# Kernel optimization log

Hardware: AMD Instinct MI355X
Metric: run time of the kernel (lower is better)

Reference implementation:

```python
import jax, jax.numpy as jnp
import numpy as np

EMBED = 128
HIDDEN = 256
N_NODES = 50000
N_EDGES = 640000
LN_EPS = 1e-5


def setup_inputs() -> dict:
    key = jax.random.key(0)
    ks = jax.random.split(key, 10)
    node_embeddings = jax.random.normal(ks[0], (N_NODES, EMBED), dtype=jnp.float32)
    edge_embeddings = jax.random.normal(ks[1], (N_EDGES, EMBED), dtype=jnp.float32)
    edge_index_list = jax.random.randint(ks[2], (2, N_EDGES), 0, N_NODES, dtype=jnp.int64 if jax.config.jax_enable_x64 else jnp.int32)
    # LayerNorm params
    ln_gamma = jnp.ones((EMBED,), dtype=jnp.float32)
    ln_beta = jnp.zeros((EMBED,), dtype=jnp.float32)
    # phi: Linear(embed->hidden), Linear(hidden->embed); xavier-ish init
    W1 = jax.random.normal(ks[3], (EMBED, HIDDEN), dtype=jnp.float32) * (1.0 / np.sqrt(EMBED))
    b1 = jnp.zeros((HIDDEN,), dtype=jnp.float32)
    W2 = jax.random.normal(ks[4], (HIDDEN, EMBED), dtype=jnp.float32) * (1.0 / np.sqrt(HIDDEN))
    b2 = jnp.zeros((EMBED,), dtype=jnp.float32)
    # theta: Linear(embed->embed)
    Wt = jax.random.normal(ks[5], (EMBED, EMBED), dtype=jnp.float32) * (1.0 / np.sqrt(EMBED))
    bt = jnp.zeros((EMBED,), dtype=jnp.float32)
    return {
        "node_embeddings": node_embeddings,
        "edge_embeddings": edge_embeddings,
        "edge_index_list": edge_index_list,
        "ln_gamma": ln_gamma, "ln_beta": ln_beta,
        "W1": W1, "b1": b1, "W2": W2, "b2": b2,
        "Wt": Wt, "bt": bt,
    }


def _layer_norm(x, gamma, beta):
    mu = jnp.mean(x, axis=-1, keepdims=True)
    var = jnp.var(x, axis=-1, keepdims=True)
    return (x - mu) * jax.lax.rsqrt(var + LN_EPS) * gamma + beta


def reference(node_embeddings, edge_embeddings, edge_index_list,
              ln_gamma, ln_beta, W1, b1, W2, b2, Wt, bt):
    n_nodes = node_embeddings.shape[0]
    h = _layer_norm(node_embeddings, ln_gamma, ln_beta)  # [N, D]
    center = edge_index_list[0]    # [E]
    neighbor = edge_index_list[1]  # [E]
    h_c = h[center]                # [E, D] gather
    h_n = h[neighbor]              # [E, D] gather
    s = edge_embeddings + h_c + h_n  # [E, D]
    # phi: SiLU -> Linear -> SiLU -> Linear
    t = jax.nn.silu(s) @ W1 + b1          # [E, H]
    theta_edge = jax.nn.silu(t) @ W2 + b2  # [E, D]
    msg = h_n * theta_edge                 # [E, D]
    agg = jax.ops.segment_sum(msg, center, num_segments=n_nodes)  # [N, D]
    # theta: SiLU -> Linear
    out = jax.nn.silu(h + agg) @ Wt + bt   # [N, D]
    return out
```

## Files before the change

kernel.cpp:

```cpp
#include <hip/hip_runtime.h>
#include <stdint.h>

#define EMBED 128
#define HIDDEN 256

typedef __bf16 v8bf __attribute__((ext_vector_type(8)));
typedef float v4f __attribute__((ext_vector_type(4)));

__device__ __forceinline__ float bf2f(unsigned short u){
    union { uint32_t i; float f; } v; v.i = ((uint32_t)u) << 16; return v.f;
}
__device__ __forceinline__ unsigned short f2bf(float f){
    union { float f; uint32_t i; } v; v.f = f;
    uint32_t i = v.i;
    uint32_t r = (i + 0x7fffu + ((i >> 16) & 1u)) >> 16;
    return (unsigned short)r;
}
__device__ __forceinline__ float lo_f(uint32_t u){ union{uint32_t i;float f;}v; v.i=u<<16; return v.f; }
__device__ __forceinline__ float hi_f(uint32_t u){ union{uint32_t i;float f;}v; v.i=u&0xffff0000u; return v.f; }
__device__ __forceinline__ uint32_t pack2(float a, float b){
    return (uint32_t)f2bf(a) | ((uint32_t)f2bf(b) << 16);
}
__device__ __forceinline__ float silu_f(float x){ return x / (1.0f + __expf(-x)); }

__device__ __forceinline__ float loadf(const void* b, size_t i, int isf32){
    return isf32 ? ((const float*)b)[i] : bf2f(((const unsigned short*)b)[i]);
}
__device__ __forceinline__ void load8f(const void* base, size_t off, int isf32, float o[8]){
    if (isf32){
        const float* p = (const float*)base + off;
        float4 a = *(const float4*)p, b = *(const float4*)(p + 4);
        o[0]=a.x;o[1]=a.y;o[2]=a.z;o[3]=a.w;o[4]=b.x;o[5]=b.y;o[6]=b.z;o[7]=b.w;
    } else {
        uint4 v = *(const uint4*)((const unsigned short*)base + off);
        uint32_t w[4] = {v.x, v.y, v.z, v.w};
        #pragma unroll
        for (int q = 0; q < 4; q++){ o[2*q] = lo_f(w[q]); o[2*q+1] = hi_f(w[q]); }
    }
}
__device__ __forceinline__ int idx_c(const int* ei, int e, int is64){
    return is64 ? ei[2*(size_t)e] : ei[e];
}
__device__ __forceinline__ int idx_n(const int* ei, int e, int E, int is64){
    return is64 ? ei[2*((size_t)E + e)] : ei[(size_t)E + e];
}

__global__ __launch_bounds__(256) void probe_kernel(
    const unsigned short* __restrict__ ne, const int* __restrict__ ei, int* __restrict__ flags)
{
    __shared__ int s_badf, s_nzidx;
    if (threadIdx.x == 0){ s_badf = 0; s_nzidx = 0; }
    __syncthreads();
    int t = threadIdx.x;
    int bad = 0;
    #pragma unroll
    for (int i = 0; i < 16; i++){
        unsigned short u = ne[t * 16 + i];
        int ex = (u >> 7) & 0xFF;
        if (ex >= 0x85) bad = 1;
    }
    if (bad) atomicOr(&s_badf, 1);
    if (t < 128 && ei[2 * t + 1] != 0) atomicOr(&s_nzidx, 1);
    __syncthreads();
    if (threadIdx.x == 0){ flags[0] = s_badf; flags[1] = s_nzidx ? 0 : 1; }
}

__global__ __launch_bounds__(256) void ln_kernel(
    const void* __restrict__ x, const void* __restrict__ g, const void* __restrict__ b,
    unsigned short* __restrict__ h, int N, const int* __restrict__ flags)
{
    int isf32 = flags[0];
    int wave = threadIdx.x >> 6, lane = threadIdx.x & 63;
    int node = blockIdx.x * 4 + wave;
    if (node >= N) return;
    float x0, x1;
    if (isf32){
        float2 v = *(const float2*)((const float*)x + (size_t)node * EMBED + lane * 2);
        x0 = v.x; x1 = v.y;
    } else {
        uint32_t u = *(const uint32_t*)((const unsigned short*)x + (size_t)node * EMBED + lane * 2);
        x0 = lo_f(u); x1 = hi_f(u);
    }
    float s = x0 + x1, ss = x0 * x0 + x1 * x1;
    for (int m = 1; m < 64; m <<= 1){ s += __shfl_xor(s, m); ss += __shfl_xor(ss, m); }
    float mean = s * (1.0f / EMBED);
    float var  = ss * (1.0f / EMBED) - mean * mean;
    float rs   = rsqrtf(var + 1e-5f);
    float g0 = loadf(g, lane * 2, isf32), g1 = loadf(g, lane * 2 + 1, isf32);
    float b0 = loadf(b, lane * 2, isf32), b1v = loadf(b, lane * 2 + 1, isf32);
    float y0 = (x0 - mean) * rs * g0 + b0;
    float y1 = (x1 - mean) * rs * g1 + b1v;
    *(uint32_t*)(h + (size_t)node * EMBED + lane * 2) = pack2(y0, y1);
}

__global__ __launch_bounds__(256) void prepack_kernel(
    const void* __restrict__ W1, const void* __restrict__ W2, const void* __restrict__ Wt,
    const void* __restrict__ b1, const void* __restrict__ b2, const void* __restrict__ bt,
    unsigned short* __restrict__ W1p, unsigned short* __restrict__ W2p,
    unsigned short* __restrict__ Wtp, unsigned short* __restrict__ bpk,
    const int* __restrict__ flags)
{
    int isf32 = flags[0];
    int t = blockIdx.x * blockDim.x + threadIdx.x;
    if (t < 32768){
        int j = t & 7, lane = (t >> 3) & 63, k32 = (t >> 9) & 3, nt = t >> 11;
        int k = k32 * 32 + (lane >> 4) * 8 + j, n = nt * 16 + (lane & 15);
        W1p[t] = f2bf(loadf(W1, (size_t)k * HIDDEN + n, isf32));
    } else if (t < 65536){
        int t2 = t - 32768;
        int j = t2 & 7, lane = (t2 >> 3) & 63, k32 = (t2 >> 9) & 7, nt = t2 >> 12;
        int k = k32 * 32 + (lane >> 4) * 8 + j, n = nt * 16 + (lane & 15);
        W2p[t2] = f2bf(loadf(W2, (size_t)k * EMBED + n, isf32));
    } else if (t < 81920){
        int t3 = t - 65536;
        int j = t3 & 7, lane = (t3 >> 3) & 63, k32 = (t3 >> 9) & 3, nt = t3 >> 11;
        int k = k32 * 32 + (lane >> 4) * 8 + j, n = nt * 16 + (lane & 15);
        Wtp[t3] = f2bf(loadf(Wt, (size_t)k * EMBED + n, isf32));
    } else if (t < 82176){
        int i = t - 81920; bpk[i] = f2bf(loadf(b1, i, isf32));
    } else if (t < 82304){
        int i = t - 82176; bpk[256 + i] = f2bf(loadf(b2, i, isf32));
    } else if (t < 82432){
        int i = t - 82304; bpk[384 + i] = f2bf(loadf(bt, i, isf32));
    }
}

__global__ __launch_bounds__(256, 3) void edge_kernel(
    const void* __restrict__ ee, const unsigned short* __restrict__ h,
    const int* __restrict__ eidx, int E,
    const unsigned short* __restrict__ W1p, const unsigned short* __restrict__ W2p,
    const unsigned short* __restrict__ bpk,
    float* __restrict__ agg, const int* __restrict__ flags)
{
    __shared__ __align__(16) unsigned short sbuf[64][136];
    __shared__ __align__(16) unsigned short tbuf[64][264];
    __shared__ int cbuf[64], nbuf[64];
    int isf32 = flags[0], is64 = flags[1];
    int wave = threadIdx.x >> 6, lane = threadIdx.x & 63;
    int quad = lane >> 4, l16 = lane & 15;
    int ebase = blockIdx.x * 64;
    int colg = l16 * 8;

    #pragma unroll
    for (int i = 0; i < 4; i++){
        int row = wave * 16 + i * 4 + quad;
        int e = ebase + row; if (e >= E) e = E - 1;
        int c = idx_c(eidx, e, is64), n = idx_n(eidx, e, E, is64);
        if (l16 == 0){ cbuf[row] = c; nbuf[row] = n; }
        float fe[8];
        load8f(ee, (size_t)e * EMBED + colg, isf32, fe);
        uint4 vc = *(const uint4*)(h + (size_t)c * EMBED + colg);
        uint4 vn = *(const uint4*)(h + (size_t)n * EMBED + colg);
        uint32_t pc[4] = {vc.x, vc.y, vc.z, vc.w};
        uint32_t pn[4] = {vn.x, vn.y, vn.z, vn.w};
        uint32_t o[4];
        #pragma unroll
        for (int q = 0; q < 4; q++){
            float a0 = fe[2*q]   + lo_f(pc[q]) + lo_f(pn[q]);
            float a1 = fe[2*q+1] + hi_f(pc[q]) + hi_f(pn[q]);
            o[q] = pack2(silu_f(a0), silu_f(a1));
        }
        *(uint4*)&sbuf[row][colg] = make_uint4(o[0], o[1], o[2], o[3]);
    }
    __syncthreads();

    {
        int ntb = wave * 4;
        v8bf bw[4][4];
        float bias[4];
        #pragma unroll
        for (int j = 0; j < 4; j++){
            bias[j] = bf2f(bpk[(ntb + j) * 16 + l16]);
            #pragma unroll
            for (int k32 = 0; k32 < 4; k32++)
                bw[j][k32] = *(const v8bf*)(W1p + ((size_t)((ntb + j) * 4 + k32) * 64 + lane) * 8);
        }
        #pragma unroll
        for (int rt = 0; rt < 4; rt++){
            v8bf a[4];
            #pragma unroll
            for (int k32 = 0; k32 < 4; k32++)
                a[k32] = *(const v8bf*)&sbuf[rt * 16 + l16][k32 * 32 + quad * 8];
            v4f acc[4];
            #pragma unroll
            for (int j = 0; j < 4; j++) acc[j] = (v4f){bias[j], bias[j], bias[j], bias[j]};
            #pragma unroll
            for (int k32 = 0; k32 < 4; k32++)
                #pragma unroll
                for (int j = 0; j < 4; j++)
                    acc[j] = __builtin_amdgcn_mfma_f32_16x16x32_bf16(a[k32], bw[j][k32], acc[j], 0, 0, 0);
            #pragma unroll
            for (int j = 0; j < 4; j++)
                #pragma unroll
                for (int r = 0; r < 4; r++)
                    tbuf[rt * 16 + quad * 4 + r][(ntb + j) * 16 + l16] = f2bf(silu_f(acc[j][r]));
        }
    }
    __syncthreads();

    {
        int ntb = wave * 2;
        v8bf bw[2][8];
        float bias[2];
        #pragma unroll
        for (int j = 0; j < 2; j++){
            bias[j] = bf2f(bpk[256 + (ntb + j) * 16 + l16]);
            #pragma unroll
            for (int k32 = 0; k32 < 8; k32++)
                bw[j][k32] = *(const v8bf*)(W2p + ((size_t)((ntb + j) * 8 + k32) * 64 + lane) * 8);
        }
        #pragma unroll
        for (int rt = 0; rt < 4; rt++){
            v8bf a[8];
            #pragma unroll
            for (int k32 = 0; k32 < 8; k32++)
                a[k32] = *(const v8bf*)&tbuf[rt * 16 + l16][k32 * 32 + quad * 8];
            v4f acc[2];
            #pragma unroll
            for (int j = 0; j < 2; j++) acc[j] = (v4f){bias[j], bias[j], bias[j], bias[j]};
            #pragma unroll
            for (int k32 = 0; k32 < 8; k32++)
                #pragma unroll
                for (int j = 0; j < 2; j++)
                    acc[j] = __builtin_amdgcn_mfma_f32_16x16x32_bf16(a[k32], bw[j][k32], acc[j], 0, 0, 0);
            #pragma unroll
            for (int j = 0; j < 2; j++){
                int col = (ntb + j) * 16 + l16;
                #pragma unroll
                for (int r = 0; r < 4; r++){
                    int row = rt * 16 + quad * 4 + r;
                    int e = ebase + row;
                    if (e < E){
                        int c = cbuf[row], n = nbuf[row];
                        float hn = bf2f(h[(size_t)n * EMBED + col]);
                        atomicAdd(&agg[(size_t)c * EMBED + col], acc[j][r] * hn);
                    }
                }
            }
        }
    }
}

__global__ __launch_bounds__(256) void node_out_kernel(
    const unsigned short* __restrict__ h, const float* __restrict__ agg,
    const unsigned short* __restrict__ Wtp, const unsigned short* __restrict__ bpk,
    void* __restrict__ out, int N, const int* __restrict__ flags)
{
    __shared__ __align__(16) unsigned short ubuf[4][16][136];
    int isf32 = flags[0];
    int wave = threadIdx.x >> 6, lane = threadIdx.x & 63;
    int quad = lane >> 4, l16 = lane & 15;
    int nbase = (blockIdx.x * 4 + wave) * 16;
    int colg = l16 * 8;
    #pragma unroll
    for (int i = 0; i < 4; i++){
        int row = i * 4 + quad;
        int node = nbase + row; int nn = node < N ? node : N - 1;
        uint4 vh = *(const uint4*)(h + (size_t)nn * EMBED + colg);
        float4 a0 = *(const float4*)(agg + (size_t)nn * EMBED + colg);
        float4 a1 = *(const float4*)(agg + (size_t)nn * EMBED + colg + 4);
        uint32_t ph[4] = {vh.x, vh.y, vh.z, vh.w};
        float af[8] = {a0.x, a0.y, a0.z, a0.w, a1.x, a1.y, a1.z, a1.w};
        uint32_t o[4];
        #pragma unroll
        for (int q = 0; q < 4; q++){
            float u0 = lo_f(ph[q]) + af[2 * q];
            float u1 = hi_f(ph[q]) + af[2 * q + 1];
            o[q] = pack2(silu_f(u0), silu_f(u1));
        }
        *(uint4*)&ubuf[wave][row][colg] = make_uint4(o[0], o[1], o[2], o[3]);
    }
    __syncthreads();
    for (int nt = 0; nt < 8; nt++){
        int col = nt * 16 + l16;
        float bc = bf2f(bpk[384 + col]);
        v4f acc = {bc, bc, bc, bc};
        #pragma unroll
        for (int k32 = 0; k32 < 4; k32++){
            v8bf a = *(const v8bf*)&ubuf[wave][l16][k32 * 32 + quad * 8];
            v8bf b = *(const v8bf*)(Wtp + ((size_t)(nt * 4 + k32) * 64 + lane) * 8);
            acc = __builtin_amdgcn_mfma_f32_16x16x32_bf16(a, b, acc, 0, 0, 0);
        }
        #pragma unroll
        for (int r = 0; r < 4; r++){
            int node = nbase + quad * 4 + r;
            if (node < N){
                if (isf32) ((float*)out)[(size_t)node * EMBED + col] = acc[r];
                else ((unsigned short*)out)[(size_t)node * EMBED + col] = f2bf(acc[r]);
            }
        }
    }
}

extern "C" void kernel_launch(void* const* d_in, const int* in_sizes, int n_in,
                              void* d_out, int out_size, void* d_ws, size_t ws_size,
                              hipStream_t stream)
{
    const void* ne = d_in[0];
    const void* ee = d_in[1];
    const int* eidx = (const int*)d_in[2];
    const void* g  = d_in[3];
    const void* be = d_in[4];
    const void* W1 = d_in[5];
    const void* b1 = d_in[6];
    const void* W2 = d_in[7];
    const void* b2 = d_in[8];
    const void* Wt = d_in[9];
    const void* bt = d_in[10];
    int N = in_sizes[0] / EMBED;
    int E = in_sizes[2] / 2;

    char* ws = (char*)d_ws;
    int* flags = (int*)ws;
    unsigned short* h = (unsigned short*)(ws + 256);
    size_t off1 = 256 + (size_t)N * EMBED * 2;
    float* agg = (float*)(ws + off1);
    size_t off2 = off1 + (size_t)N * EMBED * 4;
    unsigned short* W1p = (unsigned short*)(ws + off2);
    unsigned short* W2p = W1p + 32768;
    unsigned short* Wtp = W2p + 32768;
    unsigned short* bpk = Wtp + 16384;

    probe_kernel<<<1, 256, 0, stream>>>((const unsigned short*)ne, eidx, flags);
    hipMemsetAsync(agg, 0, (size_t)N * EMBED * sizeof(float), stream);
    prepack_kernel<<<(82432 + 255) / 256, 256, 0, stream>>>(W1, W2, Wt, b1, b2, bt,
                                                            W1p, W2p, Wtp, bpk, flags);
    ln_kernel<<<(N + 3) / 4, 256, 0, stream>>>(ne, g, be, h, N, flags);
    edge_kernel<<<(E + 63) / 64, 256, 0, stream>>>(ee, h, eidx, E,
                                                   W1p, W2p, bpk, agg, flags);
    node_out_kernel<<<(N + 63) / 64, 256, 0, stream>>>(h, agg, Wtp, bpk,
                                                       d_out, N, flags);
}
```

Baseline: 857.1 us.

## Split edge MLP hidden dim into halves, fuse probe and memset into kernels

After: 782.9 us. 8.7% less time.

```diff
diff --git a/kernel.cpp b/kernel.cpp
--- a/kernel.cpp
+++ b/kernel.cpp
@@ -1,4 +1,5 @@
 #include <hip/hip_runtime.h>
+#include <hip/hip_bf16.h>
 #include <stdint.h>
 
 #define EMBED 128
@@ -11,17 +12,18 @@
     union { uint32_t i; float f; } v; v.i = ((uint32_t)u) << 16; return v.f;
 }
 __device__ __forceinline__ unsigned short f2bf(float f){
-    union { float f; uint32_t i; } v; v.f = f;
-    uint32_t i = v.i;
-    uint32_t r = (i + 0x7fffu + ((i >> 16) & 1u)) >> 16;
-    return (unsigned short)r;
+    __hip_bfloat16 b = __float2bfloat16(f);
+    union { __hip_bfloat16 b; unsigned short u; } cv; cv.b = b; return cv.u;
+}
+__device__ __forceinline__ uint32_t pack2(float a, float b){
+    __hip_bfloat162 t = __float22bfloat162_rn(make_float2(a, b));
+    union { __hip_bfloat162 v; uint32_t u; } cv; cv.v = t; return cv.u;
 }
 __device__ __forceinline__ float lo_f(uint32_t u){ union{uint32_t i;float f;}v; v.i=u<<16; return v.f; }
 __device__ __forceinline__ float hi_f(uint32_t u){ union{uint32_t i;float f;}v; v.i=u&0xffff0000u; return v.f; }
-__device__ __forceinline__ uint32_t pack2(float a, float b){
-    return (uint32_t)f2bf(a) | ((uint32_t)f2bf(b) << 16);
-}
-__device__ __forceinline__ float silu_f(float x){ return x / (1.0f + __expf(-x)); }
+__device__ __forceinline__ float silu_f(float x){
+    return x * __builtin_amdgcn_rcpf(1.0f + __expf(-x));
+}
 
 __device__ __forceinline__ float loadf(const void* b, size_t i, int isf32){
     return isf32 ? ((const float*)b)[i] : bf2f(((const unsigned short*)b)[i]);
@@ -45,34 +47,26 @@
     return is64 ? ei[2*((size_t)E + e)] : ei[(size_t)E + e];
 }
 
-__global__ __launch_bounds__(256) void probe_kernel(
-    const unsigned short* __restrict__ ne, const int* __restrict__ ei, int* __restrict__ flags)
-{
-    __shared__ int s_badf, s_nzidx;
-    if (threadIdx.x == 0){ s_badf = 0; s_nzidx = 0; }
-    __syncthreads();
-    int t = threadIdx.x;
-    int bad = 0;
-    #pragma unroll
-    for (int i = 0; i < 16; i++){
-        unsigned short u = ne[t * 16 + i];
-        int ex = (u >> 7) & 0xFF;
-        if (ex >= 0x85) bad = 1;
-    }
-    if (bad) atomicOr(&s_badf, 1);
-    if (t < 128 && ei[2 * t + 1] != 0) atomicOr(&s_nzidx, 1);
-    __syncthreads();
-    if (threadIdx.x == 0){ flags[0] = s_badf; flags[1] = s_nzidx ? 0 : 1; }
+__device__ __forceinline__ int probe_isf32(const void* p, int lane){
+    const unsigned short* u = (const unsigned short*)p;
+    unsigned short a = u[lane], b = u[64 + lane];
+    int bad = (((a >> 7) & 0xFF) >= 0x85) | (((b >> 7) & 0xFF) >= 0x85);
+    return __any(bad) ? 1 : 0;
+}
+__device__ __forceinline__ int probe_is64(const int* ei, int lane){
+    int nz = (ei[2*lane + 1] != 0) | (ei[2*(64 + lane) + 1] != 0);
+    return __any(nz) ? 0 : 1;
 }
 
 __global__ __launch_bounds__(256) void ln_kernel(
     const void* __restrict__ x, const void* __restrict__ g, const void* __restrict__ b,
-    unsigned short* __restrict__ h, int N, const int* __restrict__ flags)
-{
-    int isf32 = flags[0];
+    unsigned short* __restrict__ h, float* __restrict__ agg, int N)
+{
     int wave = threadIdx.x >> 6, lane = threadIdx.x & 63;
+    int isf32 = probe_isf32(x, lane);
     int node = blockIdx.x * 4 + wave;
     if (node >= N) return;
+    *(float2*)(agg + (size_t)node * EMBED + lane * 2) = make_float2(0.f, 0.f);
     float x0, x1;
     if (isf32){
         float2 v = *(const float2*)((const float*)x + (size_t)node * EMBED + lane * 2);
@@ -97,10 +91,9 @@
     const void* __restrict__ W1, const void* __restrict__ W2, const void* __restrict__ Wt,
     const void* __restrict__ b1, const void* __restrict__ b2, const void* __restrict__ bt,
     unsigned short* __restrict__ W1p, unsigned short* __restrict__ W2p,
-    unsigned short* __restrict__ Wtp, unsigned short* __restrict__ bpk,
-    const int* __restrict__ flags)
-{
-    int isf32 = flags[0];
+    unsigned short* __restrict__ Wtp, unsigned short* __restrict__ bpk)
+{
+    int isf32 = probe_isf32(W1, threadIdx.x & 63);
     int t = blockIdx.x * blockDim.x + threadIdx.x;
     if (t < 32768){
         int j = t & 7, lane = (t >> 3) & 63, k32 = (t >> 9) & 3, nt = t >> 11;
@@ -116,8 +109,10 @@
         int j = t3 & 7, lane = (t3 >> 3) & 63, k32 = (t3 >> 9) & 3, nt = t3 >> 11;
         int k = k32 * 32 + (lane >> 4) * 8 + j, n = nt * 16 + (lane & 15);
         Wtp[t3] = f2bf(loadf(Wt, (size_t)k * EMBED + n, isf32));
+    } else if (t < 82048){
+        int i = t - 81920; bpk[i] = f2bf(loadf(b1, i, isf32));
     } else if (t < 82176){
-        int i = t - 81920; bpk[i] = f2bf(loadf(b1, i, isf32));
+        int i = t - 82048; bpk[128 + i] = f2bf(loadf(b1, 128 + i, isf32));
     } else if (t < 82304){
         int i = t - 82176; bpk[256 + i] = f2bf(loadf(b2, i, isf32));
     } else if (t < 82432){
@@ -125,19 +120,20 @@
     }
 }
 
-__global__ __launch_bounds__(256, 3) void edge_kernel(
+__global__ __launch_bounds__(256, 4) void edge_kernel(
     const void* __restrict__ ee, const unsigned short* __restrict__ h,
     const int* __restrict__ eidx, int E,
     const unsigned short* __restrict__ W1p, const unsigned short* __restrict__ W2p,
     const unsigned short* __restrict__ bpk,
-    float* __restrict__ agg, const int* __restrict__ flags)
+    float* __restrict__ agg)
 {
     __shared__ __align__(16) unsigned short sbuf[64][136];
-    __shared__ __align__(16) unsigned short tbuf[64][264];
+    __shared__ __align__(16) unsigned short tbuf[64][136];
     __shared__ int cbuf[64], nbuf[64];
-    int isf32 = flags[0], is64 = flags[1];
     int wave = threadIdx.x >> 6, lane = threadIdx.x & 63;
     int quad = lane >> 4, l16 = lane & 15;
+    int isf32 = probe_isf32(ee, lane);
+    int is64  = probe_is64(eidx, lane);
     int ebase = blockIdx.x * 64;
     int colg = l16 * 8;
 
@@ -164,77 +160,89 @@
     }
     __syncthreads();
 
+    v4f acc2[4][2];
     {
-        int ntb = wave * 4;
-        v8bf bw[4][4];
-        float bias[4];
-        #pragma unroll
-        for (int j = 0; j < 4; j++){
-            bias[j] = bf2f(bpk[(ntb + j) * 16 + l16]);
-            #pragma unroll
-            for (int k32 = 0; k32 < 4; k32++)
-                bw[j][k32] = *(const v8bf*)(W1p + ((size_t)((ntb + j) * 4 + k32) * 64 + lane) * 8);
-        }
-        #pragma unroll
-        for (int rt = 0; rt < 4; rt++){
-            v8bf a[4];
-            #pragma unroll
-            for (int k32 = 0; k32 < 4; k32++)
-                a[k32] = *(const v8bf*)&sbuf[rt * 16 + l16][k32 * 32 + quad * 8];
-            v4f acc[4];
-            #pragma unroll
-            for (int j = 0; j < 4; j++) acc[j] = (v4f){bias[j], bias[j], bias[j], bias[j]};
-            #pragma unroll
-            for (int k32 = 0; k32 < 4; k32++)
-                #pragma unroll
-                for (int j = 0; j < 4; j++)
-                    acc[j] = __builtin_amdgcn_mfma_f32_16x16x32_bf16(a[k32], bw[j][k32], acc[j], 0, 0, 0);
-            #pragma unroll
-            for (int j = 0; j < 4; j++)
-                #pragma unroll
-                for (int r = 0; r < 4; r++)
-                    tbuf[rt * 16 + quad * 4 + r][(ntb + j) * 16 + l16] = f2bf(silu_f(acc[j][r]));
-        }
-    }
-    __syncthreads();
-
-    {
-        int ntb = wave * 2;
-        v8bf bw[2][8];
-        float bias[2];
-        #pragma unroll
-        for (int j = 0; j < 2; j++){
-            bias[j] = bf2f(bpk[256 + (ntb + j) * 16 + l16]);
-            #pragma unroll
-            for (int k32 = 0; k32 < 8; k32++)
-                bw[j][k32] = *(const v8bf*)(W2p + ((size_t)((ntb + j) * 8 + k32) * 64 + lane) * 8);
-        }
-        #pragma unroll
-        for (int rt = 0; rt < 4; rt++){
-            v8bf a[8];
-            #pragma unroll
-            for (int k32 = 0; k32 < 8; k32++)
-                a[k32] = *(const v8bf*)&tbuf[rt * 16 + l16][k32 * 32 + quad * 8];
-            v4f acc[2];
-            #pragma unroll
-            for (int j = 0; j < 2; j++) acc[j] = (v4f){bias[j], bias[j], bias[j], bias[j]};
-            #pragma unroll
-            for (int k32 = 0; k32 < 8; k32++)
+        float bias2[2];
+        #pragma unroll
+        for (int j = 0; j < 2; j++) bias2[j] = bf2f(bpk[256 + (wave * 2 + j) * 16 + l16]);
+        #pragma unroll
+        for (int rt = 0; rt < 4; rt++)
+            #pragma unroll
+            for (int j = 0; j < 2; j++)
+                acc2[rt][j] = (v4f){bias2[j], bias2[j], bias2[j], bias2[j]};
+    }
+
+    #pragma unroll
+    for (int hf = 0; hf < 2; hf++){
+        {
+            int ntb = hf * 8 + wave * 2;
+            v8bf bw[2][4];
+            float bias[2];
+            #pragma unroll
+            for (int j = 0; j < 2; j++){
+                bias[j] = bf2f(bpk[(ntb + j) * 16 + l16]);
+                #pragma unroll
+                for (int k32 = 0; k32 < 4; k32++)
+                    bw[j][k32] = *(const v8bf*)(W1p + ((size_t)((ntb + j) * 4 + k32) * 64 + lane) * 8);
+            }
+            #pragma unroll
+            for (int rt = 0; rt < 4; rt++){
+                v8bf a[4];
+                #pragma unroll
+                for (int k32 = 0; k32 < 4; k32++)
+                    a[k32] = *(const v8bf*)&sbuf[rt * 16 + l16][k32 * 32 + quad * 8];
+                v4f acc[2];
+                #pragma unroll
+                for (int j = 0; j < 2; j++) acc[j] = (v4f){bias[j], bias[j], bias[j], bias[j]};
+                #pragma unroll
+                for (int k32 = 0; k32 < 4; k32++)
+                    #pragma unroll
+                    for (int j = 0; j < 2; j++)
+                        acc[j] = __builtin_amdgcn_mfma_f32_16x16x32_bf16(a[k32], bw[j][k32], acc[j], 0, 0, 0);
                 #pragma unroll
                 for (int j = 0; j < 2; j++)
-                    acc[j] = __builtin_amdgcn_mfma_f32_16x16x32_bf16(a[k32], bw[j][k32], acc[j], 0, 0, 0);
-            #pragma unroll
-            for (int j = 0; j < 2; j++){
-                int col = (ntb + j) * 16 + l16;
-                #pragma unroll
-                for (int r = 0; r < 4; r++){
-                    int row = rt * 16 + quad * 4 + r;
-                    int e = ebase + row;
-                    if (e < E){
-                        int c = cbuf[row], n = nbuf[row];
-                        float hn = bf2f(h[(size_t)n * EMBED + col]);
-                        atomicAdd(&agg[(size_t)c * EMBED + col], acc[j][r] * hn);
-                    }
+                    #pragma unroll
+                    for (int r = 0; r < 4; r++)
+                        tbuf[rt * 16 + quad * 4 + r][(wave * 2 + j) * 16 + l16] = f2bf(silu_f(acc[j][r]));
+            }
+        }
+        __syncthreads();
+        {
+            v8bf bw2[2][4];
+            #pragma unroll
+            for (int j = 0; j < 2; j++)
+                #pragma unroll
+                for (int kk = 0; kk < 4; kk++)
+                    bw2[j][kk] = *(const v8bf*)(W2p + ((size_t)((wave * 2 + j) * 8 + hf * 4 + kk) * 64 + lane) * 8);
+            #pragma unroll
+            for (int rt = 0; rt < 4; rt++){
+                v8bf a[4];
+                #pragma unroll
+                for (int kk = 0; kk < 4; kk++)
+                    a[kk] = *(const v8bf*)&tbuf[rt * 16 + l16][kk * 32 + quad * 8];
+                #pragma unroll
+                for (int kk = 0; kk < 4; kk++)
+                    #pragma unroll
+                    for (int j = 0; j < 2; j++)
+                        acc2[rt][j] = __builtin_amdgcn_mfma_f32_16x16x32_bf16(a[kk], bw2[j][kk], acc2[rt][j], 0, 0, 0);
+            }
+        }
+        if (hf == 0) __syncthreads();
+    }
+
+    #pragma unroll
+    for (int rt = 0; rt < 4; rt++){
+        #pragma unroll
+        for (int r = 0; r < 4; r++){
+            int row = rt * 16 + quad * 4 + r;
+            int e = ebase + row;
+            if (e < E){
+                int c = cbuf[row], n = nbuf[row];
+                #pragma unroll
+                for (int j = 0; j < 2; j++){
+                    int col = (wave * 2 + j) * 16 + l16;
+                    float hn = bf2f(h[(size_t)n * EMBED + col]);
+                    atomicAdd(&agg[(size_t)c * EMBED + col], acc2[rt][j][r] * hn);
                 }
             }
         }
@@ -242,13 +250,14 @@
 }
 
 __global__ __launch_bounds__(256) void node_out_kernel(
+    const void* __restrict__ ne,
     const unsigned short* __restrict__ h, const float* __restrict__ agg,
     const unsigned short* __restrict__ Wtp, const unsigned short* __restrict__ bpk,
-    void* __restrict__ out, int N, const int* __restrict__ flags)
+    void* __restrict__ out, int N)
 {
     __shared__ __align__(16) unsigned short ubuf[4][16][136];
-    int isf32 = flags[0];
     int wave = threadIdx.x >> 6, lane = threadIdx.x & 63;
+    int isf32 = probe_isf32(ne, lane);
     int quad = lane >> 4, l16 = lane & 15;
     int nbase = (blockIdx.x * 4 + wave) * 16;
     int colg = l16 * 8;
@@ -311,23 +320,18 @@
     int E = in_sizes[2] / 2;
 
     char* ws = (char*)d_ws;
-    int* flags = (int*)ws;
-    unsigned short* h = (unsigned short*)(ws + 256);
-    size_t off1 = 256 + (size_t)N * EMBED * 2;
-    float* agg = (float*)(ws + off1);
-    size_t off2 = off1 + (size_t)N * EMBED * 4;
-    unsigned short* W1p = (unsigned short*)(ws + off2);
+    unsigned short* h = (unsigned short*)ws;
+    float* agg = (float*)(ws + (size_t)N * EMBED * 2);
+    unsigned short* W1p = (unsigned short*)(ws + (size_t)N * EMBED * 2 + (size_t)N * EMBED * 4);
     unsigned short* W2p = W1p + 32768;
     unsigned short* Wtp = W2p + 32768;
     unsigned short* bpk = Wtp + 16384;
 
-    probe_kernel<<<1, 256, 0, stream>>>((const unsigned short*)ne, eidx, flags);
-    hipMemsetAsync(agg, 0, (size_t)N * EMBED * sizeof(float), stream);
     prepack_kernel<<<(82432 + 255) / 256, 256, 0, stream>>>(W1, W2, Wt, b1, b2, bt,
-                                                            W1p, W2p, Wtp, bpk, flags);
-    ln_kernel<<<(N + 3) / 4, 256, 0, stream>>>(ne, g, be, h, N, flags);
+                                                            W1p, W2p, Wtp, bpk);
+    ln_kernel<<<(N + 3) / 4, 256, 0, stream>>>(ne, g, be, h, agg, N);
     edge_kernel<<<(E + 63) / 64, 256, 0, stream>>>(ee, h, eidx, E,
-                                                   W1p, W2p, bpk, agg, flags);
-    node_out_kernel<<<(N + 63) / 64, 256, 0, stream>>>(h, agg, Wtp, bpk,
-                                                       d_out, N, flags);
-}
+                                                   W1p, W2p, bpk, agg);
+    node_out_kernel<<<(N + 63) / 64, 256, 0, stream>>>(ne, h, agg, Wtp, bpk,
+                                                       d_out, N);
+}
```
